# Performance work log

Measured on AMD Instinct MI355X. Metric: run time of the kernel, lower is better.

Reference implementation:

```python
import jax, jax.numpy as jnp
import numpy as np

T = 20.0
SCALE = 0.3


def setup_inputs() -> dict:
    key = jax.random.key(0)
    k1, k2, k3 = jax.random.split(key, 3)
    N, C = 65536, 1000
    outputs1 = jax.random.normal(k1, (N, C), dtype=jnp.float32)
    outputs2 = jax.random.normal(k2, (N, C), dtype=jnp.float32)
    targets = jax.random.randint(k3, (N,), 0, C, dtype=jnp.int64)
    return {"outputs1": outputs1, "outputs2": outputs2, "targets": targets}


def reference(outputs1, outputs2, targets):
    # temperature softmax over classes
    p1 = jax.nn.softmax(outputs1 / T, axis=1)  # [N, C]
    p2 = jax.nn.softmax(outputs2 / T, axis=1)  # [N, C]
    # mean-center each row
    vx = p1 - jnp.mean(p1, axis=1, keepdims=True)
    vy = p2 - jnp.mean(p2, axis=1, keepdims=True)
    # per-row Pearson correlation
    num = jnp.sum(vx * vy, axis=1)
    den = jnp.sqrt(jnp.sum(vx * vx, axis=1)) * jnp.sqrt(jnp.sum(vy * vy, axis=1))
    cost = num / den  # [N]
    return jnp.mean(SCALE * cost)
```

## Files before the change

kernel.cpp:

```cpp
#include <hip/hip_runtime.h>


#define N_ROWS 65536
#define N_C    1000
#define N_C4   250
#define S1_BLOCKS 2048
#define WAVES_PER_BLOCK 4

__device__ __forceinline__ double wave_reduce_add(double v) {
    #pragma unroll
    for (int off = 32; off > 0; off >>= 1)
        v += __shfl_down(v, off, 64);
    return v;
}

__global__ __launch_bounds__(256) void div2_stage1(
        const float* __restrict__ o1, const float* __restrict__ o2,
        double* __restrict__ ws) {
    const int wave = threadIdx.x >> 6;
    const int lane = threadIdx.x & 63;
    const int gwave = blockIdx.x * WAVES_PER_BLOCK + wave;
    const int nwaves = gridDim.x * WAVES_PER_BLOCK;

    constexpr float INV_T = 1.0f / 20.0f;
    double acc = 0.0;

    for (int row = gwave; row < N_ROWS; row += nwaves) {
        const float4* r1 = reinterpret_cast<const float4*>(o1 + (size_t)row * N_C);
        const float4* r2 = reinterpret_cast<const float4*>(o2 + (size_t)row * N_C);
        double sx = 0.0, sy = 0.0, sxx = 0.0, syy = 0.0, sxy = 0.0;
        for (int j = lane; j < N_C4; j += 64) {
            float4 a = r1[j];
            float4 b = r2[j];
            #pragma unroll
            for (int k = 0; k < 4; ++k) {
                float av = (k == 0) ? a.x : (k == 1) ? a.y : (k == 2) ? a.z : a.w;
                float bv = (k == 0) ? b.x : (k == 1) ? b.y : (k == 2) ? b.z : b.w;
                float xf = __expf(av * INV_T);
                float yf = __expf(bv * INV_T);
                double x = (double)xf, y = (double)yf;
                sx += x;  sy += y;
                sxx = fma(x, x, sxx);
                syy = fma(y, y, syy);
                sxy = fma(x, y, sxy);
            }
        }
        sx  = wave_reduce_add(sx);
        sy  = wave_reduce_add(sy);
        sxx = wave_reduce_add(sxx);
        syy = wave_reduce_add(syy);
        sxy = wave_reduce_add(sxy);
        if (lane == 0) {
            constexpr double invC = 1.0 / (double)N_C;
            double num = sxy - sx * sy * invC;
            double vx  = sxx - sx * sx * invC;
            double vy  = syy - sy * sy * invC;
            acc += num / sqrt(vx * vy);
        }
    }

    __shared__ double lds[WAVES_PER_BLOCK];
    if (lane == 0) lds[wave] = acc;
    __syncthreads();
    if (threadIdx.x == 0) {
        double s = 0.0;
        #pragma unroll
        for (int w = 0; w < WAVES_PER_BLOCK; ++w) s += lds[w];
        ws[blockIdx.x] = s;
    }
}

__global__ __launch_bounds__(256) void div2_stage2(
        const double* __restrict__ ws, int n, float* __restrict__ out) {
    double s = 0.0;
    for (int i = threadIdx.x; i < n; i += 256) s += ws[i];
    s = wave_reduce_add(s);
    __shared__ double lds[4];
    const int wave = threadIdx.x >> 6;
    const int lane = threadIdx.x & 63;
    if (lane == 0) lds[wave] = s;
    __syncthreads();
    if (threadIdx.x == 0) {
        double t = lds[0] + lds[1] + lds[2] + lds[3];
        out[0] = (float)(t * (0.3 / (double)N_ROWS));
    }
}

extern "C" void kernel_launch(void* const* d_in, const int* in_sizes, int n_in,
                              void* d_out, int out_size, void* d_ws, size_t ws_size,
                              hipStream_t stream) {
    const float* o1 = (const float*)d_in[0];
    const float* o2 = (const float*)d_in[1];
    float* out = (float*)d_out;
    double* ws = (double*)d_ws;

    int nblocks = S1_BLOCKS;
    size_t need = (size_t)nblocks * sizeof(double);
    if (ws_size < need) {
        nblocks = (int)(ws_size / sizeof(double));
        if (nblocks < 1) nblocks = 1;
    }

    div2_stage1<<<nblocks, 256, 0, stream>>>(o1, o2, ws);
    div2_stage2<<<1, 256, 0, stream>>>(ws, nblocks, out);
}
```

Baseline: 100.7 us.

## Double-buffer rows into LDS via async global loads and accumulate in float

Each wave processes a contiguous block of eight rows and prefetches the next row into a second LDS buffer with global_load_lds while it computes the current one. Per-lane sums move from double to float, using exp(x)-1 shifting to keep precision, and five reductions are interleaved with xor shuffles. The goal is to hide memory latency and cut fp64 arithmetic cost. The cost is hardcoded sizes with no workspace check, manual vmcnt waits, and somewhat reduced accumulation precision.

Measured after the change: 104.0 us. 3.3% more time.

```diff
diff --git a/kernel.cpp b/kernel.cpp
--- a/kernel.cpp
+++ b/kernel.cpp
@@ -1,80 +1,119 @@
 #include <hip/hip_runtime.h>
 
 
-#define N_ROWS 65536
-#define N_C    1000
-#define N_C4   250
-#define S1_BLOCKS 2048
-#define WAVES_PER_BLOCK 4
+#define N_ROWS   65536
+#define N_C      1000
+#define NBLOCKS  2048
+#define WPB      4
+#define RPW      8
 
-__device__ __forceinline__ double wave_reduce_add(double v) {
+__device__ __forceinline__ void gload16(const float* g, float* s) {
+    __builtin_amdgcn_global_load_lds(
+        (const __attribute__((address_space(1))) void*)g,
+        (__attribute__((address_space(3))) void*)s, 16, 0, 0);
+}
+
+__device__ __forceinline__ void stage_row(const float* __restrict__ o1,
+                                          const float* __restrict__ o2,
+                                          long row, float* dst, int lane) {
+    const float* r1 = o1 + row * (long)N_C;
+    const float* r2 = o2 + row * (long)N_C;
+    const int l4 = lane * 4;
+    gload16(r1 + l4,       dst);
+    gload16(r1 + 256 + l4, dst + 256);
+    gload16(r1 + 512 + l4, dst + 512);
+    gload16(r2 + l4,       dst + 1024);
+    gload16(r2 + 256 + l4, dst + 1280);
+    gload16(r2 + 512 + l4, dst + 1536);
+    bool tail_ok = (lane < 58) || (row + 1 < (long)N_ROWS);
+    if (tail_ok) {
+        gload16(r1 + 768 + l4, dst + 768);
+        gload16(r2 + 768 + l4, dst + 1792);
+    }
+}
+
+__device__ __forceinline__ double row_cost(const float* buf, int lane) {
+    const float4* A = reinterpret_cast<const float4*>(buf);
+    const float4* B = reinterpret_cast<const float4*>(buf + 1024);
+    constexpr float INV_T = 1.0f / 20.0f;
+    float sx = 0.f, sy = 0.f, sxx = 0.f, syy = 0.f, sxy = 0.f;
     #pragma unroll
-    for (int off = 32; off > 0; off >>= 1)
-        v += __shfl_down(v, off, 64);
-    return v;
+    for (int k = 0; k < 4; ++k) {
+        float4 a = A[k * 64 + lane];
+        float4 b = B[k * 64 + lane];
+        const bool ok = (k < 3) || (lane < 58);
+        float av[4] = {a.x, a.y, a.z, a.w};
+        float bv[4] = {b.x, b.y, b.z, b.w};
+        #pragma unroll
+        for (int e = 0; e < 4; ++e) {
+            float va = ok ? av[e] : 0.0f;
+            float vb = ok ? bv[e] : 0.0f;
+            float x = __expf(va * INV_T) - 1.0f;
+            float y = __expf(vb * INV_T) - 1.0f;
+            sx += x;  sy += y;
+            sxx = fmaf(x, x, sxx);
+            syy = fmaf(y, y, syy);
+            sxy = fmaf(x, y, sxy);
+        }
+    }
+    #pragma unroll
+    for (int off = 32; off; off >>= 1) {
+        sx  += __shfl_xor(sx,  off, 64);
+        sy  += __shfl_xor(sy,  off, 64);
+        sxx += __shfl_xor(sxx, off, 64);
+        syy += __shfl_xor(syy, off, 64);
+        sxy += __shfl_xor(sxy, off, 64);
+    }
+    constexpr double invC = 1.0 / (double)N_C;
+    double dx = (double)sx, dy = (double)sy;
+    double num = (double)sxy - dx * dy * invC;
+    double vx  = (double)sxx - dx * dx * invC;
+    double vy  = (double)syy - dy * dy * invC;
+    return num / sqrt(vx * vy);
 }
 
 __global__ __launch_bounds__(256) void div2_stage1(
         const float* __restrict__ o1, const float* __restrict__ o2,
         double* __restrict__ ws) {
+    __shared__ float lds[WPB][2][2048];
     const int wave = threadIdx.x >> 6;
     const int lane = threadIdx.x & 63;
-    const int gwave = blockIdx.x * WAVES_PER_BLOCK + wave;
-    const int nwaves = gridDim.x * WAVES_PER_BLOCK;
+    const int gw   = blockIdx.x * WPB + wave;
+    const long r0  = (long)gw * RPW;
 
-    constexpr float INV_T = 1.0f / 20.0f;
+    float* buf0 = &lds[wave][0][0];
+    float* buf1 = &lds[wave][1][0];
+
+    stage_row(o1, o2, r0, buf0, lane);
+
     double acc = 0.0;
-
-    for (int row = gwave; row < N_ROWS; row += nwaves) {
-        const float4* r1 = reinterpret_cast<const float4*>(o1 + (size_t)row * N_C);
-        const float4* r2 = reinterpret_cast<const float4*>(o2 + (size_t)row * N_C);
-        double sx = 0.0, sy = 0.0, sxx = 0.0, syy = 0.0, sxy = 0.0;
-        for (int j = lane; j < N_C4; j += 64) {
-            float4 a = r1[j];
-            float4 b = r2[j];
-            #pragma unroll
-            for (int k = 0; k < 4; ++k) {
-                float av = (k == 0) ? a.x : (k == 1) ? a.y : (k == 2) ? a.z : a.w;
-                float bv = (k == 0) ? b.x : (k == 1) ? b.y : (k == 2) ? b.z : b.w;
-                float xf = __expf(av * INV_T);
-                float yf = __expf(bv * INV_T);
-                double x = (double)xf, y = (double)yf;
-                sx += x;  sy += y;
-                sxx = fma(x, x, sxx);
-                syy = fma(y, y, syy);
-                sxy = fma(x, y, sxy);
-            }
+    #pragma unroll 1
+    for (int p = 0; p < RPW; ++p) {
+        float* cur = (p & 1) ? buf1 : buf0;
+        float* nxt = (p & 1) ? buf0 : buf1;
+        if (p + 1 < RPW) {
+            stage_row(o1, o2, r0 + p + 1, nxt, lane);
+            asm volatile("s_waitcnt vmcnt(8)" ::: "memory");
+        } else {
+            asm volatile("s_waitcnt vmcnt(0)" ::: "memory");
         }
-        sx  = wave_reduce_add(sx);
-        sy  = wave_reduce_add(sy);
-        sxx = wave_reduce_add(sxx);
-        syy = wave_reduce_add(syy);
-        sxy = wave_reduce_add(sxy);
-        if (lane == 0) {
-            constexpr double invC = 1.0 / (double)N_C;
-            double num = sxy - sx * sy * invC;
-            double vx  = sxx - sx * sx * invC;
-            double vy  = syy - sy * sy * invC;
-            acc += num / sqrt(vx * vy);
-        }
+        acc += row_cost(cur, lane);
     }
 
-    __shared__ double lds[WAVES_PER_BLOCK];
-    if (lane == 0) lds[wave] = acc;
     __syncthreads();
-    if (threadIdx.x == 0) {
-        double s = 0.0;
-        #pragma unroll
-        for (int w = 0; w < WAVES_PER_BLOCK; ++w) s += lds[w];
-        ws[blockIdx.x] = s;
-    }
+    double* dred = reinterpret_cast<double*>(&lds[0][0][0]);
+    if (lane == 0) dred[wave] = acc;
+    __syncthreads();
+    if (threadIdx.x == 0)
+        ws[blockIdx.x] = dred[0] + dred[1] + dred[2] + dred[3];
 }
 
 __global__ __launch_bounds__(256) void div2_stage2(
         const double* __restrict__ ws, int n, float* __restrict__ out) {
     double s = 0.0;
     for (int i = threadIdx.x; i < n; i += 256) s += ws[i];
-    s = wave_reduce_add(s);
+    #pragma unroll
+    for (int off = 32; off; off >>= 1) s += __shfl_xor(s, off, 64);
     __shared__ double lds[4];
     const int wave = threadIdx.x >> 6;
     const int lane = threadIdx.x & 63;
@@ -94,13 +133,6 @@
     float* out = (float*)d_out;
     double* ws = (double*)d_ws;
 
-    int nblocks = S1_BLOCKS;
-    size_t need = (size_t)nblocks * sizeof(double);
-    if (ws_size < need) {
-        nblocks = (int)(ws_size / sizeof(double));
-        if (nblocks < 1) nblocks = 1;
-    }
-
-    div2_stage1<<<nblocks, 256, 0, stream>>>(o1, o2, ws);
-    div2_stage2<<<1, 256, 0, stream>>>(ws, nblocks, out);
+    div2_stage1<<<NBLOCKS, 256, 0, stream>>>(o1, o2, ws);
+    div2_stage2<<<1, 256, 0, stream>>>(ws, NBLOCKS, out);
 }
```
